# Optimization experiments

Measured on AMD Instinct MI355X. Metric: run time of the kernel, lower is better.

The kernel has to match this reference:

```python
import jax, jax.numpy as jnp
import numpy as np

B, S, D = 2, 2048, 1024
H = 16
HD = D // H  # head_dim = 64


def setup_inputs() -> dict:
    key = jax.random.key(0)
    ks = jax.random.split(key, 9)
    sc_in = 1.0 / np.sqrt(D)
    return {
        "x": jax.random.normal(ks[0], (B, S, D), dtype=jnp.float32),
        "Wq": jax.random.normal(ks[1], (D, D), dtype=jnp.float32) * sc_in,
        "bq": jnp.zeros((D,), dtype=jnp.float32),
        "Wk": jax.random.normal(ks[2], (D, D), dtype=jnp.float32) * sc_in,
        "bk": jnp.zeros((D,), dtype=jnp.float32),
        "Wv": jax.random.normal(ks[3], (D, D), dtype=jnp.float32) * sc_in,
        "bv": jnp.zeros((D,), dtype=jnp.float32),
        "Wo": jax.random.normal(ks[4], (D, D), dtype=jnp.float32) * sc_in,
        "bo": jnp.zeros((D,), dtype=jnp.float32),
    }


def reference(x, Wq, bq, Wk, bk, Wv, bv, Wo, bo):
    # QKV projections: [B,S,D] -> [B,H,S,HD]
    def split_heads(t):
        return t.reshape(B, S, H, HD).transpose(0, 2, 1, 3)

    Q = split_heads(x @ Wq + bq)
    K = split_heads(x @ Wk + bk)
    V = split_heads(x @ Wv + bv)

    scale = 1.0 / np.sqrt(HD).astype(np.float32)
    scores = jnp.einsum("bhqd,bhkd->bhqk", Q, K) * scale  # [B,H,S,S]
    weights = jax.nn.softmax(scores, axis=-1)
    # dropout(p=0.1) is identity in eval mode
    attended = jnp.einsum("bhqk,bhkd->bhqd", weights, V)  # [B,H,S,HD]
    attended = attended.transpose(0, 2, 1, 3).reshape(B, S, D)
    return attended @ Wo + bo
```

## Files before the change

### kernel.cpp

```cpp
#include <hip/hip_runtime.h>
#include <hip/hip_bf16.h>


#define S_ 2048
#define D_ 1024
#define HD_ 64
#define LDSW 72
#define QSZ 4194304

typedef __attribute__((ext_vector_type(8))) short bf16x8;
typedef __attribute__((ext_vector_type(4))) float f32x4;

static __device__ __forceinline__ short f2bs(float f) {
    __hip_bfloat16 h = __float2bfloat16(f);
    return *reinterpret_cast<short*>(&h);
}
static __device__ __forceinline__ float bs2f(short s) {
    __hip_bfloat16 h = *reinterpret_cast<__hip_bfloat16*>(&s);
    return __bfloat162float(h);
}
static __device__ __forceinline__ bf16x8 cvt8(const float* p) {
    f32x4 u0 = *(const f32x4*)p;
    f32x4 u1 = *(const f32x4*)(p + 4);
    bf16x8 r;
    r[0] = f2bs(u0[0]); r[1] = f2bs(u0[1]); r[2] = f2bs(u0[2]); r[3] = f2bs(u0[3]);
    r[4] = f2bs(u1[0]); r[5] = f2bs(u1[1]); r[6] = f2bs(u1[2]); r[7] = f2bs(u1[3]);
    return r;
}
static __device__ __forceinline__ void gld16(const void* g, void* l) {
    __builtin_amdgcn_global_load_lds(
        (const __attribute__((address_space(1))) unsigned int*)g,
        (__attribute__((address_space(3))) unsigned int*)l, 16, 0, 0);
}
static __device__ __forceinline__ int detect_f32(const unsigned int* __restrict__ xw) {
    const unsigned int w = xw[threadIdx.x & 63];
    const int e = (int)((w >> 7) & 0xFFu);
    unsigned long long m = __ballot(e >= 117 && e <= 130);
    return (__popcll(m) >= 32) ? 0 : 1;
}

__global__ __launch_bounds__(256) void prep(
    const void* __restrict__ x,
    const void* __restrict__ w0, const void* __restrict__ w1,
    const void* __restrict__ w2, const void* __restrict__ w3,
    short* __restrict__ Wt)
{
    __shared__ __align__(16) short Ts[64 * LDSW];
    const int f32in = detect_f32((const unsigned int*)x);
    const int idx = blockIdx.x;
    const int z = idx >> 8, bb = idx & 255;
    const void* W = z == 0 ? w0 : z == 1 ? w1 : z == 2 ? w2 : w3;
    short* O = Wt + (size_t)z * D_ * D_;
    const int k0 = (bb & 15) * 64, n0 = (bb >> 4) * 64;
    const int t = threadIdx.x;
    const int row = t >> 2, seg = t & 3;

    if (f32in) {
        const float* wg = (const float*)W + (size_t)(k0 + row) * D_ + n0;
        *(bf16x8*)&Ts[row * LDSW + seg * 8]      = cvt8(wg + seg * 8);
        *(bf16x8*)&Ts[row * LDSW + seg * 8 + 32] = cvt8(wg + seg * 8 + 32);
    } else {
        const short* wg = (const short*)W + (size_t)(k0 + row) * D_ + n0;
        *(bf16x8*)&Ts[row * LDSW + seg * 8]      = *(const bf16x8*)(wg + seg * 8);
        *(bf16x8*)&Ts[row * LDSW + seg * 8 + 32] = *(const bf16x8*)(wg + seg * 8 + 32);
    }
    __syncthreads();

    short* og = O + (size_t)(n0 + row) * D_ + k0;
    #pragma unroll
    for (int g = 0; g < 2; ++g) {
        const int ks = seg * 8 + g * 32;
        alignas(16) short tmp[8];
        #pragma unroll
        for (int i = 0; i < 8; ++i) tmp[i] = Ts[(ks + i) * LDSW + row];
        *(bf16x8*)(og + ks) = *(const bf16x8*)tmp;
    }
}

__global__ __launch_bounds__(256) void gemm_qkv(
    const void* __restrict__ X, const short* __restrict__ Wt3,
    const void* __restrict__ bq, const void* __restrict__ bk,
    const void* __restrict__ bv, short* __restrict__ out)
{
    __shared__ __align__(16) short As[128 * 64];
    __shared__ __align__(16) short Bs[128 * 64];
    const int ext_f32 = detect_f32((const unsigned int*)X);
    const int t = threadIdx.x;
    const int wave = t >> 6, lane = t & 63;
    const int quad = lane >> 4, l16 = lane & 15;
    const int wm = wave & 1, wn = wave >> 1;
    const int m0 = blockIdx.x * 128, n0 = blockIdx.y * 128;
    const int id = n0 >> 10;
    const int lr = lane >> 3;
    const int kx = ((lane & 7) ^ (lr & 7)) * 8;

    f32x4 acc[4][4];
    #pragma unroll
    for (int i = 0; i < 4; ++i)
        #pragma unroll
        for (int j = 0; j < 4; ++j) acc[i][j] = (f32x4){0.f, 0.f, 0.f, 0.f};

    const size_t arow = (size_t)(m0 + wave * 32 + lr) * D_ + kx;
    const short* Bb = Wt3 + (size_t)(n0 + wave * 32 + lr) * D_ + kx;

    for (int kb = 0; kb < 16; ++kb) {
        __syncthreads();
        const int k0 = kb * 64;
        if (ext_f32) {
            const float* Xf = (const float*)X;
            #pragma unroll
            for (int i = 0; i < 4; ++i)
                *(bf16x8*)&As[(wave * 4 + i) * 512 + lane * 8] =
                    cvt8(Xf + arow + (size_t)i * 8 * D_ + k0);
        } else {
            const short* Xs = (const short*)X;
            #pragma unroll
            for (int i = 0; i < 4; ++i)
                gld16(Xs + arow + (size_t)i * 8 * D_ + k0, &As[(wave * 4 + i) * 512]);
        }
        #pragma unroll
        for (int i = 0; i < 4; ++i)
            gld16(Bb + (size_t)i * 8 * D_ + k0, &Bs[(wave * 4 + i) * 512]);
        __syncthreads();

        #pragma unroll
        for (int ks = 0; ks < 2; ++ks) {
            const int sw = ((ks * 4 + quad) ^ (l16 & 7)) * 8;
            bf16x8 af[4], bfr[4];
            #pragma unroll
            for (int i = 0; i < 4; ++i) {
                af[i]  = *(const bf16x8*)&As[(wm * 64 + i * 16 + l16) * 64 + sw];
                bfr[i] = *(const bf16x8*)&Bs[(wn * 64 + i * 16 + l16) * 64 + sw];
            }
            #pragma unroll
            for (int mi = 0; mi < 4; ++mi)
                #pragma unroll
                for (int ni = 0; ni < 4; ++ni)
                    acc[mi][ni] = __builtin_amdgcn_mfma_f32_16x16x32_bf16(
                        af[mi], bfr[ni], acc[mi][ni], 0, 0, 0);
        }
    }

    const void* bias = id == 0 ? bq : id == 1 ? bk : bv;
    const float oscale = id == 0 ? 0.18033688011112042f : 1.0f;
    #pragma unroll
    for (int ni = 0; ni < 4; ++ni) {
        const int n = n0 + wn * 64 + ni * 16 + l16;
        const int nl = n & 1023, h = nl >> 6, d = nl & 63;
        const float bvl = ext_f32 ? ((const float*)bias)[nl]
                                  : bs2f(((const short*)bias)[nl]);
        #pragma unroll
        for (int mi = 0; mi < 4; ++mi)
            #pragma unroll
            for (int r = 0; r < 4; ++r) {
                const int m = m0 + wm * 64 + mi * 16 + quad * 4 + r;
                const int b = m >> 11, s = m & 2047;
                const int bh = b * 16 + h;
                const float v = (acc[mi][ni][r] + bvl) * oscale;
                const size_t idx = (id < 2)
                    ? (size_t)id * QSZ + ((size_t)bh * S_ + s) * HD_ + d
                    : (size_t)2 * QSZ + ((size_t)bh * HD_ + d) * S_ + s;
                out[idx] = f2bs(v);
            }
    }
}

__global__ __launch_bounds__(256) void gemm_out(
    const short* __restrict__ A, const short* __restrict__ Bt,
    const void* __restrict__ bias, void* __restrict__ C,
    const unsigned int* __restrict__ xw)
{
    __shared__ __align__(16) short As[64 * 64];
    __shared__ __align__(16) short Bs[128 * 64];
    const int ext_f32 = detect_f32(xw);
    const int t = threadIdx.x;
    const int wave = t >> 6, lane = t & 63;
    const int quad = lane >> 4, l16 = lane & 15;
    const int wm = wave & 1, wn = wave >> 1;
    const int m0 = blockIdx.x * 64, n0 = blockIdx.y * 128;
    const int lr = lane >> 3;
    const int kx = ((lane & 7) ^ (lr & 7)) * 8;

    f32x4 acc[2][4];
    #pragma unroll
    for (int i = 0; i < 2; ++i)
        #pragma unroll
        for (int j = 0; j < 4; ++j) acc[i][j] = (f32x4){0.f, 0.f, 0.f, 0.f};

    const short* Ab = A  + (size_t)(m0 + wave * 16 + lr) * D_ + kx;
    const short* Bb = Bt + (size_t)(n0 + wave * 32 + lr) * D_ + kx;

    for (int kb = 0; kb < 16; ++kb) {
        __syncthreads();
        const int k0 = kb * 64;
        #pragma unroll
        for (int i = 0; i < 2; ++i)
            gld16(Ab + (size_t)i * 8 * D_ + k0, &As[(wave * 2 + i) * 512]);
        #pragma unroll
        for (int i = 0; i < 4; ++i)
            gld16(Bb + (size_t)i * 8 * D_ + k0, &Bs[(wave * 4 + i) * 512]);
        __syncthreads();

        #pragma unroll
        for (int ks = 0; ks < 2; ++ks) {
            const int sw = ((ks * 4 + quad) ^ (l16 & 7)) * 8;
            bf16x8 af[2], bfr[4];
            #pragma unroll
            for (int i = 0; i < 2; ++i)
                af[i] = *(const bf16x8*)&As[(wm * 32 + i * 16 + l16) * 64 + sw];
            #pragma unroll
            for (int i = 0; i < 4; ++i)
                bfr[i] = *(const bf16x8*)&Bs[(wn * 64 + i * 16 + l16) * 64 + sw];
            #pragma unroll
            for (int mi = 0; mi < 2; ++mi)
                #pragma unroll
                for (int ni = 0; ni < 4; ++ni)
                    acc[mi][ni] = __builtin_amdgcn_mfma_f32_16x16x32_bf16(
                        af[mi], bfr[ni], acc[mi][ni], 0, 0, 0);
        }
    }

    #pragma unroll
    for (int ni = 0; ni < 4; ++ni) {
        const int n = n0 + wn * 64 + ni * 16 + l16;
        const float bvl = ext_f32 ? ((const float*)bias)[n]
                                  : bs2f(((const short*)bias)[n]);
        #pragma unroll
        for (int mi = 0; mi < 2; ++mi)
            #pragma unroll
            for (int r = 0; r < 4; ++r) {
                const int m = m0 + wm * 32 + mi * 16 + quad * 4 + r;
                const float v = acc[mi][ni][r] + bvl;
                const size_t idx = (size_t)m * D_ + n;
                if (ext_f32) ((float*)C)[idx] = v;
                else         ((short*)C)[idx] = f2bs(v);
            }
    }
}

__global__ __launch_bounds__(512) void attn(
    const short* __restrict__ Q, const short* __restrict__ K,
    const short* __restrict__ Vt, short* __restrict__ Aout)
{
    __shared__ __align__(16) short Ks[2][64 * 64];
    __shared__ __align__(16) short Vs[2][64 * 64];
    __shared__ __align__(16) short Ps[8][16 * LDSW];

    const int t = threadIdx.x;
    const int wave = t >> 6, lane = t & 63;
    const int quad = lane >> 4, l16 = lane & 15;
    const int bh = blockIdx.x;
    const int q0 = blockIdx.y * 128;
    const int lr = lane >> 3;
    const int kx = ((lane & 7) ^ (lr & 7)) * 8;
    short* pw = &Ps[wave][0];

    bf16x8 bq0, bq1;
    {
        const short* qr = Q + ((size_t)bh * S_ + q0 + wave * 16 + l16) * HD_ + quad * 8;
        bq0 = *(const bf16x8*)qr;
        bq1 = *(const bf16x8*)(qr + 32);
    }

    bf16x8 ones;
    #pragma unroll
    for (int i = 0; i < 8; ++i) ones[i] = (short)0x3F80;

    f32x4 o[4], lacc;
    lacc = (f32x4){0.f, 0.f, 0.f, 0.f};
    #pragma unroll
    for (int nt = 0; nt < 4; ++nt) o[nt] = (f32x4){0.f, 0.f, 0.f, 0.f};

    const short* Kb = K  + ((size_t)bh * S_  + wave * 8 + lr) * HD_ + kx;
    const short* Vb = Vt + ((size_t)bh * HD_ + wave * 8 + lr) * S_ + kx;

    gld16(Kb, &Ks[0][wave * 512]);
    gld16(Vb, &Vs[0][wave * 512]);
    __syncthreads();

    for (int j = 0; j < 32; ++j) {
        const int cur = j & 1;
        if (j < 31) {
            gld16(Kb + (size_t)((j + 1) * 64) * HD_, &Ks[cur ^ 1][wave * 512]);
            gld16(Vb + (j + 1) * 64,                 &Vs[cur ^ 1][wave * 512]);
        }

        f32x4 st[4];
        #pragma unroll
        for (int nt = 0; nt < 4; ++nt) {
            bf16x8 kf0 = *(const bf16x8*)&Ks[cur][(nt * 16 + l16) * 64 + ((quad ^ (l16 & 7)) * 8)];
            bf16x8 kf1 = *(const bf16x8*)&Ks[cur][(nt * 16 + l16) * 64 + (((4 + quad) ^ (l16 & 7)) * 8)];
            f32x4 z = (f32x4){0.f, 0.f, 0.f, 0.f};
            z = __builtin_amdgcn_mfma_f32_16x16x32_bf16(kf0, bq0, z, 0, 0, 0);
            z = __builtin_amdgcn_mfma_f32_16x16x32_bf16(kf1, bq1, z, 0, 0, 0);
            st[nt] = z;
        }

        #pragma unroll
        for (int nt = 0; nt < 4; ++nt) {
            unsigned u0 = __float_as_uint(__builtin_amdgcn_exp2f(st[nt][0]));
            unsigned u1 = __float_as_uint(__builtin_amdgcn_exp2f(st[nt][1]));
            unsigned u2 = __float_as_uint(__builtin_amdgcn_exp2f(st[nt][2]));
            unsigned u3 = __float_as_uint(__builtin_amdgcn_exp2f(st[nt][3]));
            uint2 pk;
            pk.x = __builtin_amdgcn_perm(u1, u0, 0x07060302);
            pk.y = __builtin_amdgcn_perm(u3, u2, 0x07060302);
            *(uint2*)&pw[l16 * LDSW + nt * 16 + quad * 4] = pk;
        }
        __builtin_amdgcn_s_waitcnt(0xc07f);

        #pragma unroll
        for (int ks = 0; ks < 2; ++ks) {
            bf16x8 vf[4];
            #pragma unroll
            for (int nt = 0; nt < 4; ++nt)
                vf[nt] = *(const bf16x8*)&Vs[cur][(nt * 16 + l16) * 64 + (((ks * 4 + quad) ^ (l16 & 7)) * 8)];
            bf16x8 ap = *(const bf16x8*)&pw[l16 * LDSW + ks * 32 + quad * 8];
            lacc = __builtin_amdgcn_mfma_f32_16x16x32_bf16(ap, ones, lacc, 0, 0, 0);
            #pragma unroll
            for (int nt = 0; nt < 4; ++nt)
                o[nt] = __builtin_amdgcn_mfma_f32_16x16x32_bf16(ap, vf[nt], o[nt], 0, 0, 0);
        }

        __syncthreads();
    }

    const int b = bh >> 4, h = bh & 15;
    #pragma unroll
    for (int r = 0; r < 4; ++r) {
        const float inv = 1.f / lacc[r];
        const int s = q0 + wave * 16 + quad * 4 + r;
        const size_t base = ((size_t)b * S_ + s) * D_ + h * HD_;
        #pragma unroll
        for (int nt = 0; nt < 4; ++nt)
            Aout[base + nt * 16 + l16] = f2bs(o[nt][r] * inv);
    }
}

extern "C" void kernel_launch(void* const* d_in, const int* in_sizes, int n_in,
                              void* d_out, int out_size, void* d_ws, size_t ws_size,
                              hipStream_t stream) {
    char* ws = (char*)d_ws;
    short* Wt  = (short*)(ws + ((size_t)1  << 20));
    short* Att = (short*)(ws + ((size_t)9  << 20));
    short* QKV = (short*)(ws + ((size_t)17 << 20));
    const unsigned int* xw = (const unsigned int*)d_in[0];

    prep<<<1024, 256, 0, stream>>>(d_in[0], d_in[1], d_in[3], d_in[5], d_in[7], Wt);
    gemm_qkv<<<dim3(32, 24), 256, 0, stream>>>(d_in[0], Wt, d_in[2], d_in[4], d_in[6], QKV);
    attn<<<dim3(32, 16), 512, 0, stream>>>(QKV, QKV + QSZ, QKV + 2 * QSZ, Att);
    gemm_out<<<dim3(64, 8), 256, 0, stream>>>(Att, Wt + (3 << 20), d_in[8], d_out, xw);
}
```

Before: 188.8 us.

## Triple-buffer K/V tiles in attention with partial vmcnt waits and priority hints

The attention kernel moves from double to triple buffering of K/V tiles in LDS, prefetching two tiles ahead. It replaces __syncthreads with a partial vmcnt wait plus a raw barrier, so one load group can stay in flight across the barrier. All K and V fragments are loaded up front each iteration, and the MFMA sections are wrapped in s_setprio. It also adds a launch-bounds occupancy hint. The cost is more LDS per block, which may lower occupancy, plus wasted wrap-around prefetches on the last two iterations.

```diff
diff --git a/kernel.cpp b/kernel.cpp
--- a/kernel.cpp
+++ b/kernel.cpp
@@ -238,12 +238,12 @@
     }
 }
 
-__global__ __launch_bounds__(512) void attn(
+__global__ __launch_bounds__(512, 4) void attn(
     const short* __restrict__ Q, const short* __restrict__ K,
     const short* __restrict__ Vt, short* __restrict__ Aout)
 {
-    __shared__ __align__(16) short Ks[2][64 * 64];
-    __shared__ __align__(16) short Vs[2][64 * 64];
+    __shared__ __align__(16) short Ks[3][64 * 64];
+    __shared__ __align__(16) short Vs[3][64 * 64];
     __shared__ __align__(16) short Ps[8][16 * LDSW];
 
     const int t = threadIdx.x;
@@ -274,27 +274,47 @@
     const short* Kb = K  + ((size_t)bh * S_  + wave * 8 + lr) * HD_ + kx;
     const short* Vb = Vt + ((size_t)bh * HD_ + wave * 8 + lr) * S_ + kx;
 
-    gld16(Kb, &Ks[0][wave * 512]);
-    gld16(Vb, &Vs[0][wave * 512]);
-    __syncthreads();
-
+    gld16(Kb,                   &Ks[0][wave * 512]);
+    gld16(Vb,                   &Vs[0][wave * 512]);
+    gld16(Kb + (size_t)64 * HD_, &Ks[1][wave * 512]);
+    gld16(Vb + 64,               &Vs[1][wave * 512]);
+    asm volatile("s_waitcnt vmcnt(2)" ::: "memory");
+    __builtin_amdgcn_sched_barrier(0);
+    __builtin_amdgcn_s_barrier();
+
+    int cur = 0;
     for (int j = 0; j < 32; ++j) {
-        const int cur = j & 1;
-        if (j < 31) {
-            gld16(Kb + (size_t)((j + 1) * 64) * HD_, &Ks[cur ^ 1][wave * 512]);
-            gld16(Vb + (j + 1) * 64,                 &Vs[cur ^ 1][wave * 512]);
-        }
+        const int pre = cur == 0 ? 2 : cur - 1;
+        const int jn = (j + 2) & 31;
+        gld16(Kb + (size_t)(jn * 64) * HD_, &Ks[pre][wave * 512]);
+        gld16(Vb + jn * 64,                 &Vs[pre][wave * 512]);
+
+        const short* Kc = &Ks[cur][0];
+        const short* Vc = &Vs[cur][0];
+
+        bf16x8 kf[4][2];
+        #pragma unroll
+        for (int nt = 0; nt < 4; ++nt) {
+            kf[nt][0] = *(const bf16x8*)&Kc[(nt * 16 + l16) * 64 + ((quad ^ (l16 & 7)) * 8)];
+            kf[nt][1] = *(const bf16x8*)&Kc[(nt * 16 + l16) * 64 + (((4 + quad) ^ (l16 & 7)) * 8)];
+        }
+        bf16x8 vf[2][4];
+        #pragma unroll
+        for (int ks = 0; ks < 2; ++ks)
+            #pragma unroll
+            for (int nt = 0; nt < 4; ++nt)
+                vf[ks][nt] = *(const bf16x8*)&Vc[(nt * 16 + l16) * 64 + (((ks * 4 + quad) ^ (l16 & 7)) * 8)];
 
         f32x4 st[4];
+        __builtin_amdgcn_s_setprio(1);
         #pragma unroll
         for (int nt = 0; nt < 4; ++nt) {
-            bf16x8 kf0 = *(const bf16x8*)&Ks[cur][(nt * 16 + l16) * 64 + ((quad ^ (l16 & 7)) * 8)];
-            bf16x8 kf1 = *(const bf16x8*)&Ks[cur][(nt * 16 + l16) * 64 + (((4 + quad) ^ (l16 & 7)) * 8)];
             f32x4 z = (f32x4){0.f, 0.f, 0.f, 0.f};
-            z = __builtin_amdgcn_mfma_f32_16x16x32_bf16(kf0, bq0, z, 0, 0, 0);
-            z = __builtin_amdgcn_mfma_f32_16x16x32_bf16(kf1, bq1, z, 0, 0, 0);
+            z = __builtin_amdgcn_mfma_f32_16x16x32_bf16(kf[nt][0], bq0, z, 0, 0, 0);
+            z = __builtin_amdgcn_mfma_f32_16x16x32_bf16(kf[nt][1], bq1, z, 0, 0, 0);
             st[nt] = z;
         }
+        __builtin_amdgcn_s_setprio(0);
 
         #pragma unroll
         for (int nt = 0; nt < 4; ++nt) {
@@ -309,20 +329,23 @@
         }
         __builtin_amdgcn_s_waitcnt(0xc07f);
 
+        __builtin_amdgcn_s_setprio(1);
         #pragma unroll
         for (int ks = 0; ks < 2; ++ks) {
-            bf16x8 vf[4];
-            #pragma unroll
-            for (int nt = 0; nt < 4; ++nt)
-                vf[nt] = *(const bf16x8*)&Vs[cur][(nt * 16 + l16) * 64 + (((ks * 4 + quad) ^ (l16 & 7)) * 8)];
             bf16x8 ap = *(const bf16x8*)&pw[l16 * LDSW + ks * 32 + quad * 8];
             lacc = __builtin_amdgcn_mfma_f32_16x16x32_bf16(ap, ones, lacc, 0, 0, 0);
             #pragma unroll
             for (int nt = 0; nt < 4; ++nt)
-                o[nt] = __builtin_amdgcn_mfma_f32_16x16x32_bf16(ap, vf[nt], o[nt], 0, 0, 0);
-        }
-
-        __syncthreads();
+                o[nt] = __builtin_amdgcn_mfma_f32_16x16x32_bf16(ap, vf[ks][nt], o[nt], 0, 0, 0);
+        }
+        __builtin_amdgcn_s_setprio(0);
+
+        asm volatile("s_waitcnt vmcnt(2)" ::: "memory");
+        __builtin_amdgcn_sched_barrier(0);
+        __builtin_amdgcn_s_barrier();
+        __builtin_amdgcn_sched_barrier(0);
+
+        cur = cur == 2 ? 0 : cur + 1;
     }
 
     const int b = bh >> 4, h = bh & 15;
```

Result: no change. 191.0 us (+1.2%).
